# Kernel tuning notes

Hardware: AMD Instinct MI355X
Metric: run time of the kernel (lower is better)

## Reference

```python
import jax, jax.numpy as jnp
import numpy as np

D_MODEL = 1024
N_HEADS = 16
SEQ = 512  # == max_seq_len; rel-pos bias requires n_token == max_seq_len


def setup_inputs() -> dict:
    key = jax.random.key(0)
    ks = jax.random.split(key, 12)
    B = 16
    x = jax.random.normal(ks[0], (B, SEQ, D_MODEL), dtype=jnp.float32)
    c = jax.random.normal(ks[1], (B, SEQ, 8), dtype=jnp.float32)  # unused by forward
    s = 1.0 / np.sqrt(D_MODEL)
    Wq = jax.random.normal(ks[2], (D_MODEL, D_MODEL), dtype=jnp.float32) * s
    bq = jnp.zeros((D_MODEL,), dtype=jnp.float32)
    Wk = jax.random.normal(ks[3], (D_MODEL, D_MODEL), dtype=jnp.float32) * s
    bk = jnp.zeros((D_MODEL,), dtype=jnp.float32)
    Wv = jax.random.normal(ks[4], (D_MODEL, D_MODEL), dtype=jnp.float32) * s
    bv = jnp.zeros((D_MODEL,), dtype=jnp.float32)
    Wo = jax.random.normal(ks[5], (D_MODEL, D_MODEL), dtype=jnp.float32) * s
    bo = jnp.zeros((D_MODEL,), dtype=jnp.float32)
    # trunc_normal_(std=0.02) approximated by normal*0.02 (values stay small)
    rel_table = jax.random.normal(ks[6], (2 * SEQ - 1, N_HEADS), dtype=jnp.float32) * 0.02
    return {"x": x, "c": c, "Wq": Wq, "bq": bq, "Wk": Wk, "bk": bk,
            "Wv": Wv, "bv": bv, "Wo": Wo, "bo": bo, "rel_table": rel_table}


def reference(x, c, Wq, bq, Wk, bk, Wv, bv, Wo, bo, rel_table):
    # x: [B, S, D]; c is unused in the original forward
    B, S, D = x.shape
    H = N_HEADS
    dk = D // H
    scale = 1.0 / np.sqrt(dk)

    q = (x @ Wq + bq).reshape(B, S, H, dk)
    k = (x @ Wk + bk).reshape(B, S, H, dk)
    v = (x @ Wv + bv).reshape(B, S, H, dk)

    # scores: [B, H, S, S]
    scores = jnp.einsum('bihd,bjhd->bhij', q, k) * scale

    # relative position bias: index[i,j] = i + (S-1-j), values in [0, 2S-2]
    rel_index = jnp.arange(S)[:, None] + jnp.arange(S - 1, -1, -1)[None, :]  # [S,S]
    bias = rel_table[rel_index]            # [S, S, H]
    scores = scores + jnp.transpose(bias, (2, 0, 1))[None]  # [1,H,S,S]

    # causal_mask=False: original adds False * -1e9 == 0, so no mask term
    probs = jax.nn.softmax(scores, axis=-1)

    out = jnp.einsum('bhij,bjhd->bihd', probs, v).reshape(B, S, D)
    return out @ Wo + bo
```

## Files before the change

kernel.cpp:

```cpp
#include <hip/hip_runtime.h>
#include <hip/hip_bf16.h>
#include <stdint.h>

#define D_MODEL 1024
#define NH 16
#define SEQ 512
#define DK 64
#define BATCH 16
#define M_TOT (BATCH*SEQ)

typedef unsigned short u16;
typedef unsigned int u32;
typedef __attribute__((ext_vector_type(8))) __bf16 bf16x8;
typedef __attribute__((ext_vector_type(4))) u16 ushort4v;
typedef __attribute__((ext_vector_type(4))) float f32x4;

static __device__ __forceinline__ u16 f2bf(float f) {
    union { float f; u32 i; } c; c.f = f;
    return (u16)((c.i + 0x8000u) >> 16);
}
static __device__ __forceinline__ void async_copy16(const void* g, void* l) {
    __builtin_amdgcn_global_load_lds(
        (const __attribute__((address_space(1))) u32*)g,
        (__attribute__((address_space(3))) u32*)l, 16, 0, 0);
}
static __device__ __forceinline__ float fexp2(float x) {
    float r; asm("v_exp_f32 %0, %1" : "=v"(r) : "v"(x)); return r;
}

__global__ __launch_bounds__(256) void prep(const float* __restrict__ x,
                                            u16* __restrict__ xbf,
                                            const float* __restrict__ Wq,
                                            const float* __restrict__ Wk,
                                            const float* __restrict__ Wv,
                                            u16* __restrict__ Wt3) {
    __shared__ u16 tile[64][65];
    const int bid = blockIdx.x;
    const int t = threadIdx.x;
    if (bid < 2048) {
        #pragma unroll
        for (int it = 0; it < 4; ++it) {
            const int i = (bid * 1024 + it * 256 + t) * 4;
            float4 v = *(const float4*)&x[i];
            ushort4v o;
            o[0] = f2bf(v.x); o[1] = f2bf(v.y); o[2] = f2bf(v.z); o[3] = f2bf(v.w);
            *(ushort4v*)&xbf[i] = o;
        }
        return;
    }
    const int tw = bid - 2048;
    const int z = tw >> 8;
    const float* W = (z == 0) ? Wq : (z == 1) ? Wk : Wv;
    const int n0 = (tw & 15) * 64, k0 = ((tw >> 4) & 15) * 64;
    #pragma unroll
    for (int p = 0; p < 16; ++p) {
        int idx = p * 256 + t;
        int r = idx >> 6, c = idx & 63;
        tile[r][c] = f2bf(W[(size_t)(k0 + r) * D_MODEL + (n0 + c)]);
    }
    __syncthreads();
    #pragma unroll
    for (int p = 0; p < 16; ++p) {
        int idx = p * 256 + t;
        int r = idx >> 6, c = idx & 63;
        Wt3[((size_t)z * D_MODEL + n0 + r) * D_MODEL + (k0 + c)] = tile[c][r];
    }
}

__global__ __launch_bounds__(256) void gemm_bt(const u16* __restrict__ A,
                                               const u16* __restrict__ Bt,
                                               const float* __restrict__ b0,
                                               const float* __restrict__ b1,
                                               const float* __restrict__ b2,
                                               void* __restrict__ o0,
                                               void* __restrict__ o1,
                                               void* __restrict__ o2,
                                               int qkv) {
    __shared__ __attribute__((aligned(16))) u16 smem[16896];
    u16* Asm = smem;
    u16* Bsm = smem + 8192;
    const int t = threadIdx.x;
    const int m0 = blockIdx.y * 128, n0 = blockIdx.x * 128;
    const int lane = t & 63, w = t >> 6;
    const int lm = lane & 15, quad = lane >> 4;
    const int wm = w >> 1, wn = w & 1;

    f32x4 acc[4][4];
    #pragma unroll
    for (int i = 0; i < 4; ++i)
        #pragma unroll
        for (int j = 0; j < 4; ++j) acc[i][j] = (f32x4){0.f, 0.f, 0.f, 0.f};

    for (int kt = 0; kt < D_MODEL / 64; ++kt) {
        const int k0 = kt * 64;
        __syncthreads();
        #pragma unroll
        for (int i = 0; i < 4; ++i) {
            int chunk = i * 256 + t;
            int row = chunk >> 3, c = chunk & 7;
            int cs = c ^ (row & 7);
            async_copy16(A + (size_t)(m0 + row) * D_MODEL + k0 + cs * 8, &Asm[chunk * 8]);
        }
        #pragma unroll
        for (int i = 0; i < 4; ++i) {
            int chunk = i * 256 + t;
            int row = chunk >> 3, c = chunk & 7;
            int cs = c ^ (row & 7);
            async_copy16(Bt + (size_t)(n0 + row) * D_MODEL + k0 + cs * 8, &Bsm[chunk * 8]);
        }
        __syncthreads();
        #pragma unroll
        for (int ks = 0; ks < 64; ks += 32) {
            const int cbase = ks >> 3;
            bf16x8 af[4], bfv[4];
            #pragma unroll
            for (int im = 0; im < 4; ++im) {
                const int row = wm * 64 + im * 16 + lm;
                const int c = (cbase + quad) ^ (row & 7);
                af[im] = *(const bf16x8*)&Asm[row * 64 + c * 8];
            }
            #pragma unroll
            for (int in = 0; in < 4; ++in) {
                const int row = wn * 64 + in * 16 + lm;
                const int c = (cbase + quad) ^ (row & 7);
                bfv[in] = *(const bf16x8*)&Bsm[row * 64 + c * 8];
            }
            #pragma unroll
            for (int im = 0; im < 4; ++im)
                #pragma unroll
                for (int in = 0; in < 4; ++in)
                    acc[im][in] = __builtin_amdgcn_mfma_f32_16x16x32_bf16(
                        af[im], bfv[in], acc[im][in], 0, 0, 0);
        }
    }

    __syncthreads();
    if (qkv) {
        const int sel = n0 >> 10;
        if (sel == 2) {
            #pragma unroll
            for (int in = 0; in < 4; ++in) {
                const int nn = (n0 & 1023) + wn * 64 + in * 16 + lm;
                const float bv = b2[nn];
                const int h = nn >> 6, d = nn & 63;
                #pragma unroll
                for (int im = 0; im < 4; ++im) {
                    const int mb = m0 + wm * 64 + im * 16 + quad * 4;
                    const int b = mb >> 9, s = mb & 511;
                    ushort4v pk;
                    #pragma unroll
                    for (int r = 0; r < 4; ++r) pk[r] = f2bf(acc[im][in][r] + bv);
                    *(ushort4v*)&((u16*)o2)[((size_t)(b * NH + h) * DK + d) * SEQ + s] = pk;
                }
            }
        } else {
            u16* dst = sel ? (u16*)o1 : (u16*)o0;
            const float* bb = sel ? b1 : b0;
            u16 (*Cs)[132] = (u16(*)[132])smem;
            #pragma unroll
            for (int in = 0; in < 4; ++in) {
                const int nl = wn * 64 + in * 16 + lm;
                const float bv = bb[(n0 & 1023) + nl];
                #pragma unroll
                for (int im = 0; im < 4; ++im)
                    #pragma unroll
                    for (int r = 0; r < 4; ++r)
                        Cs[wm * 64 + im * 16 + quad * 4 + r][nl] =
                            f2bf(acc[im][in][r] + bv);
            }
            __syncthreads();
            const int rr = t >> 1, hh = t & 1;
            const int m = m0 + rr;
            const int b = m >> 9, s = m & 511;
            const int h = ((n0 & 1023) >> 6) + hh;
            u16* dp = &dst[((size_t)(b * NH + h) * SEQ + s) * DK];
            #pragma unroll
            for (int c = 0; c < 8; ++c)
                *(uint4*)&dp[c * 8] = *(const uint4*)&Cs[rr][hh * 64 + c * 8];
        }
    } else {
        float (*Cs)[132] = (float(*)[132])smem;
        #pragma unroll
        for (int ph = 0; ph < 2; ++ph) {
            if (wm == ph) {
                #pragma unroll
                for (int in = 0; in < 4; ++in) {
                    const int nl = wn * 64 + in * 16 + lm;
                    const float bv = b0[n0 + nl];
                    #pragma unroll
                    for (int im = 0; im < 4; ++im)
                        #pragma unroll
                        for (int r = 0; r < 4; ++r)
                            Cs[im * 16 + quad * 4 + r][nl] = acc[im][in][r] + bv;
                }
            }
            __syncthreads();
            const int rr = t >> 2, qq = t & 3;
            float* dp = &((float*)o0)[(size_t)(m0 + ph * 64 + rr) * D_MODEL + n0 + qq * 32];
            #pragma unroll
            for (int c = 0; c < 8; ++c)
                *(uint4*)&dp[c * 4] = *(const uint4*)&Cs[rr][qq * 32 + c * 4];
            __syncthreads();
        }
    }
}

__global__ __launch_bounds__(256) void attn_flash(const u16* __restrict__ qg,
                                                  const u16* __restrict__ kg,
                                                  const u16* __restrict__ vTg,
                                                  const float* __restrict__ rel,
                                                  u16* __restrict__ aout,
                                                  const float* __restrict__ Wo,
                                                  u16* __restrict__ WtO) {
    __shared__ __attribute__((aligned(16))) u16 qt[128 * 64];
    __shared__ __attribute__((aligned(16))) u16 Pl[4][32][72];
    __shared__ __attribute__((aligned(16))) float bcs[4][648];

    const int t = threadIdx.x;
    const int F = blockIdx.x;
    if (F >= 1024) {
        u16 (*tile)[65] = (u16(*)[65])qt;
        const int tw = F - 1024;
        const int n0 = (tw & 15) * 64, k0 = (tw >> 4) * 64;
        #pragma unroll
        for (int p = 0; p < 16; ++p) {
            int idx = p * 256 + t;
            int r = idx >> 6, c = idx & 63;
            tile[r][c] = f2bf(Wo[(size_t)(k0 + r) * D_MODEL + (n0 + c)]);
        }
        __syncthreads();
        #pragma unroll
        for (int p = 0; p < 16; ++p) {
            int idx = p * 256 + t;
            int r = idx >> 6, c = idx & 63;
            WtO[(size_t)(n0 + r) * D_MODEL + (k0 + c)] = tile[c][r];
        }
        return;
    }

    const int lane = t & 63, w = t >> 6;
    const int lm = lane & 15, quad = lane >> 4;
    const int xcd = F & 7, qti = (F >> 3) & 3, grp = F >> 5;
    const int p = grp * 8 + xcd;
    const int h = p & 15, b = p >> 4;
    const int q0 = qti * 128;
    const size_t bh = (size_t)(b * NH + h);
    const u16* qb = qg + bh * SEQ * DK;
    const u16* kb = kg + bh * SEQ * DK;
    const u16* vb = vTg + bh * DK * SEQ;

    #pragma unroll
    for (int i = 0; i < 4; ++i) {
        const int chunk = i * 256 + t, row = chunk >> 3, c = chunk & 7;
        const int cs = c ^ (row & 7);
        *(uint4*)&qt[chunk * 8] = *(const uint4*)&qb[(q0 + row) * DK + cs * 8];
    }
    for (int u = t; u < 639; u += 256) {
        const float bv = rel[(q0 + u) * NH + h] * 1.44269504f;
        #pragma unroll
        for (int c = 0; c < 4; ++c) bcs[c][u + 4 - c] = bv;
    }

    __syncthreads();

    bf16x8 aq[2][2];
    #pragma unroll
    for (int g = 0; g < 2; ++g) {
        const int ra = w * 32 + g * 16 + lm;
        aq[g][0] = *(const bf16x8*)&qt[ra * 64 + ((quad) ^ (ra & 7)) * 8];
        aq[g][1] = *(const bf16x8*)&qt[ra * 64 + ((4 + quad) ^ (ra & 7)) * 8];
    }

    float lsum[2] = {0.f, 0.f};
    f32x4 o[2][4];
    #pragma unroll
    for (int g = 0; g < 2; ++g)
        #pragma unroll
        for (int sd = 0; sd < 4; ++sd) o[g][sd] = (f32x4){0.f, 0.f, 0.f, 0.f};

    const float scale2 = 0.125f * 1.44269504f;
    const int cc = lm & 3;
    const int abase = w * 32 + lm + 512 - quad * 4 - cc;

    for (int jt = 0; jt < 8; ++jt) {
        const int j0 = jt * 64;

        #pragma unroll
        for (int js = 0; js < 4; ++js) {
            const u16* kp = kb + (size_t)(j0 + js * 16 + lm) * DK;
            bf16x8 bk0 = *(const bf16x8*)&kp[quad * 8];
            bf16x8 bk1 = *(const bf16x8*)&kp[32 + quad * 8];
            #pragma unroll
            for (int g = 0; g < 2; ++g) {
                f32x4 c = (f32x4){0.f, 0.f, 0.f, 0.f};
                c = __builtin_amdgcn_mfma_f32_16x16x32_bf16(bk0, aq[g][0], c, 0, 0, 0);
                c = __builtin_amdgcn_mfma_f32_16x16x32_bf16(bk1, aq[g][1], c, 0, 0, 0);
                const f32x4 bc4 = *(const f32x4*)&bcs[cc][abase + g * 16 - j0 - js * 16];
                ushort4v pk;
                #pragma unroll
                for (int r = 0; r < 4; ++r) {
                    float e = fexp2(c[r] * scale2 + bc4[3 - r]);
                    lsum[g] += e;
                    pk[r] = f2bf(e);
                }
                *(ushort4v*)&Pl[w][g * 16 + lm][js * 16 + quad * 4] = pk;
            }
        }

        bf16x8 ap[2][2];
        #pragma unroll
        for (int g = 0; g < 2; ++g) {
            ap[g][0] = *(const bf16x8*)&Pl[w][g * 16 + lm][quad * 8];
            ap[g][1] = *(const bf16x8*)&Pl[w][g * 16 + lm][32 + quad * 8];
        }
        #pragma unroll
        for (int sd = 0; sd < 4; ++sd) {
            const u16* vp = vb + (size_t)(sd * 16 + lm) * SEQ + j0;
            bf16x8 bv0 = *(const bf16x8*)&vp[quad * 8];
            bf16x8 bv1 = *(const bf16x8*)&vp[32 + quad * 8];
            #pragma unroll
            for (int g = 0; g < 2; ++g) {
                o[g][sd] = __builtin_amdgcn_mfma_f32_16x16x32_bf16(bv0, ap[g][0], o[g][sd], 0, 0, 0);
                o[g][sd] = __builtin_amdgcn_mfma_f32_16x16x32_bf16(bv1, ap[g][1], o[g][sd], 0, 0, 0);
            }
        }
    }

    #pragma unroll
    for (int g = 0; g < 2; ++g) {
        float s = lsum[g];
        s += __shfl_xor(s, 16, 64);
        s += __shfl_xor(s, 32, 64);
        const float rinv = 1.0f / s;
        #pragma unroll
        for (int sd = 0; sd < 4; ++sd) {
            ushort4v pk;
            #pragma unroll
            for (int r = 0; r < 4; ++r) pk[r] = f2bf(o[g][sd][r] * rinv);
            *(ushort4v*)&Pl[w][g * 16 + lm][sd * 16 + quad * 4] = pk;
        }
    }
    const int rowl = lane >> 1, ch = lane & 1;
    u16* dp = aout + (size_t)(b * SEQ + q0 + w * 32 + rowl) * D_MODEL + h * DK + ch * 32;
    #pragma unroll
    for (int c = 0; c < 4; ++c)
        *(uint4*)&dp[c * 8] = *(const uint4*)&Pl[w][rowl][ch * 32 + c * 8];
}

extern "C" void kernel_launch(void* const* d_in, const int* in_sizes, int n_in,
                              void* d_out, int out_size, void* d_ws, size_t ws_size,
                              hipStream_t stream) {
    const float* x   = (const float*)d_in[0];
    const float* Wq  = (const float*)d_in[2];
    const float* bq  = (const float*)d_in[3];
    const float* Wk  = (const float*)d_in[4];
    const float* bk  = (const float*)d_in[5];
    const float* Wv  = (const float*)d_in[6];
    const float* bv  = (const float*)d_in[7];
    const float* Wo  = (const float*)d_in[8];
    const float* bo  = (const float*)d_in[9];
    const float* rel = (const float*)d_in[10];
    float* out = (float*)d_out;

    u16* ws = (u16*)d_ws;
    const size_t WSZ = (size_t)D_MODEL * D_MODEL;
    const size_t TSZ = (size_t)M_TOT * D_MODEL;
    u16* Wt3 = ws;
    u16* xbf = Wt3 + 3 * WSZ;
    u16* qws = xbf + TSZ;
    u16* kws = qws + TSZ;
    u16* vws = kws + TSZ;
    u16* aws = xbf;

    dim3 tb(256);
    prep<<<dim3(2048 + 768), tb, 0, stream>>>(x, xbf, Wq, Wk, Wv, Wt3);
    gemm_bt<<<dim3(24, 64), tb, 0, stream>>>(xbf, Wt3, bq, bk, bv, qws, kws, vws, 1);
    attn_flash<<<dim3(1024 + 256), tb, 0, stream>>>(qws, kws, vws, rel, aws, Wo, Wt3);
    gemm_bt<<<dim3(8, 64), tb, 0, stream>>>(aws, Wt3, bo, nullptr, nullptr,
                                            (void*)out, nullptr, nullptr, 0);
}
```

Before: 291.5 us.

## Double-buffer K/V tiles in LDS with async copies and MFMA row sums

The attention kernel now stages K and V^T tiles into double-buffered LDS with async global-to-LDS copies. The next tile is prefetched while the current one is computed, replacing direct global loads inside the inner loop. The softmax denominator is accumulated by an MFMA against a ones vector instead of scalar adds plus shuffles. Bias is stored once rather than four shifted copies, and bf16 packing uses the hardware v_cvt_pk_bf16_f32. The trade-offs are more LDS per block (possibly lower occupancy), an extra barrier per tile, and a row sum computed from bf16-rounded probabilities.

```diff
diff --git a/kernel.cpp b/kernel.cpp
--- a/kernel.cpp
+++ b/kernel.cpp
@@ -18,6 +18,9 @@
 static __device__ __forceinline__ u16 f2bf(float f) {
     union { float f; u32 i; } c; c.f = f;
     return (u16)((c.i + 0x8000u) >> 16);
+}
+static __device__ __forceinline__ u32 cvtpk(float lo, float hi) {
+    u32 r; asm("v_cvt_pk_bf16_f32 %0, %1, %2" : "=v"(r) : "v"(lo), "v"(hi)); return r;
 }
 static __device__ __forceinline__ void async_copy16(const void* g, void* l) {
     __builtin_amdgcn_global_load_lds(
@@ -212,14 +215,17 @@
                                                   u16* __restrict__ aout,
                                                   const float* __restrict__ Wo,
                                                   u16* __restrict__ WtO) {
-    __shared__ __attribute__((aligned(16))) u16 qt[128 * 64];
-    __shared__ __attribute__((aligned(16))) u16 Pl[4][32][72];
-    __shared__ __attribute__((aligned(16))) float bcs[4][648];
+    __shared__ __attribute__((aligned(16))) char smem_raw[53760];
+    u16* ktb = (u16*)smem_raw;
+    u16* vtb = (u16*)(smem_raw + 16384);
+    float* biasb = (float*)(smem_raw + 32768);
+    u16* qt = (u16*)(smem_raw + 35328);
+    u16 (*Pl)[32][72] = (u16(*)[32][72])(smem_raw + 35328);
 
     const int t = threadIdx.x;
     const int F = blockIdx.x;
     if (F >= 1024) {
-        u16 (*tile)[65] = (u16(*)[65])qt;
+        u16 (*tile)[65] = (u16(*)[65])smem_raw;
         const int tw = F - 1024;
         const int n0 = (tw & 15) * 64, k0 = (tw >> 4) * 64;
         #pragma unroll
@@ -250,16 +256,20 @@
     const u16* vb = vTg + bh * DK * SEQ;
 
     #pragma unroll
+    for (int i = 0; i < 2; ++i) {
+        const int chunk = i * 256 + t, row = chunk >> 3, c = chunk & 7;
+        const int cs = c ^ (row & 7);
+        async_copy16(kb + row * DK + cs * 8, &ktb[chunk * 8]);
+        async_copy16(vb + row * SEQ + cs * 8, &vtb[chunk * 8]);
+    }
+
+    #pragma unroll
     for (int i = 0; i < 4; ++i) {
         const int chunk = i * 256 + t, row = chunk >> 3, c = chunk & 7;
         const int cs = c ^ (row & 7);
         *(uint4*)&qt[chunk * 8] = *(const uint4*)&qb[(q0 + row) * DK + cs * 8];
     }
-    for (int u = t; u < 639; u += 256) {
-        const float bv = rel[(q0 + u) * NH + h] * 1.44269504f;
-        #pragma unroll
-        for (int c = 0; c < 4; ++c) bcs[c][u + 4 - c] = bv;
-    }
+    for (int u = t; u < 639; u += 256) biasb[u] = rel[(q0 + u) * NH + h] * 1.44269504f;
 
     __syncthreads();
 
@@ -270,40 +280,59 @@
         aq[g][0] = *(const bf16x8*)&qt[ra * 64 + ((quad) ^ (ra & 7)) * 8];
         aq[g][1] = *(const bf16x8*)&qt[ra * 64 + ((4 + quad) ^ (ra & 7)) * 8];
     }
-
-    float lsum[2] = {0.f, 0.f};
+    __syncthreads();
+
+    bf16x8 ones;
+    #pragma unroll
+    for (int i = 0; i < 8; ++i) ones[i] = (__bf16)1.0f;
+
+    f32x4 ol[2];
     f32x4 o[2][4];
     #pragma unroll
-    for (int g = 0; g < 2; ++g)
+    for (int g = 0; g < 2; ++g) {
+        ol[g] = (f32x4){0.f, 0.f, 0.f, 0.f};
         #pragma unroll
         for (int sd = 0; sd < 4; ++sd) o[g][sd] = (f32x4){0.f, 0.f, 0.f, 0.f};
+    }
 
     const float scale2 = 0.125f * 1.44269504f;
-    const int cc = lm & 3;
-    const int abase = w * 32 + lm + 512 - quad * 4 - cc;
 
     for (int jt = 0; jt < 8; ++jt) {
+        if (jt) __syncthreads();
+        const int cur = jt & 1, nxt = cur ^ 1;
+        u16* ktc = ktb + cur * 4096;
+        u16* vtc = vtb + cur * 4096;
+        if (jt < 7) {
+            const int j1 = (jt + 1) * 64;
+            u16* ktn = ktb + nxt * 4096;
+            u16* vtn = vtb + nxt * 4096;
+            #pragma unroll
+            for (int i = 0; i < 2; ++i) {
+                const int chunk = i * 256 + t, row = chunk >> 3, c = chunk & 7;
+                const int cs = c ^ (row & 7);
+                async_copy16(kb + (j1 + row) * DK + cs * 8, &ktn[chunk * 8]);
+                async_copy16(vb + row * SEQ + j1 + cs * 8, &vtn[chunk * 8]);
+            }
+        }
         const int j0 = jt * 64;
 
         #pragma unroll
         for (int js = 0; js < 4; ++js) {
-            const u16* kp = kb + (size_t)(j0 + js * 16 + lm) * DK;
-            bf16x8 bk0 = *(const bf16x8*)&kp[quad * 8];
-            bf16x8 bk1 = *(const bf16x8*)&kp[32 + quad * 8];
+            const int rb = js * 16 + lm;
+            bf16x8 bk0 = *(const bf16x8*)&ktc[rb * 64 + ((quad) ^ (rb & 7)) * 8];
+            bf16x8 bk1 = *(const bf16x8*)&ktc[rb * 64 + ((4 + quad) ^ (rb & 7)) * 8];
             #pragma unroll
             for (int g = 0; g < 2; ++g) {
                 f32x4 c = (f32x4){0.f, 0.f, 0.f, 0.f};
                 c = __builtin_amdgcn_mfma_f32_16x16x32_bf16(bk0, aq[g][0], c, 0, 0, 0);
                 c = __builtin_amdgcn_mfma_f32_16x16x32_bf16(bk1, aq[g][1], c, 0, 0, 0);
-                const f32x4 bc4 = *(const f32x4*)&bcs[cc][abase + g * 16 - j0 - js * 16];
-                ushort4v pk;
-                #pragma unroll
-                for (int r = 0; r < 4; ++r) {
-                    float e = fexp2(c[r] * scale2 + bc4[3 - r]);
-                    lsum[g] += e;
-                    pk[r] = f2bf(e);
-                }
-                *(ushort4v*)&Pl[w][g * 16 + lm][js * 16 + quad * 4] = pk;
+                const int bb0 = w * 32 + g * 16 + lm + 511 - j0 - js * 16 - quad * 4;
+                float e0 = fexp2(c[0] * scale2 + biasb[bb0]);
+                float e1 = fexp2(c[1] * scale2 + biasb[bb0 - 1]);
+                float e2 = fexp2(c[2] * scale2 + biasb[bb0 - 2]);
+                float e3 = fexp2(c[3] * scale2 + biasb[bb0 - 3]);
+                uint2 pk = {cvtpk(e0, e1), cvtpk(e2, e3)};
+                *(uint2*)&Pl[w][g * 16 + lm][js * 16 + quad * 4] = pk;
             }
         }
 
@@ -312,12 +341,14 @@
         for (int g = 0; g < 2; ++g) {
             ap[g][0] = *(const bf16x8*)&Pl[w][g * 16 + lm][quad * 8];
             ap[g][1] = *(const bf16x8*)&Pl[w][g * 16 + lm][32 + quad * 8];
+            ol[g] = __builtin_amdgcn_mfma_f32_16x16x32_bf16(ones, ap[g][0], ol[g], 0, 0, 0);
+            ol[g] = __builtin_amdgcn_mfma_f32_16x16x32_bf16(ones, ap[g][1], ol[g], 0, 0, 0);
         }
         #pragma unroll
         for (int sd = 0; sd < 4; ++sd) {
-            const u16* vp = vb + (size_t)(sd * 16 + lm) * SEQ + j0;
-            bf16x8 bv0 = *(const bf16x8*)&vp[quad * 8];
-            bf16x8 bv1 = *(const bf16x8*)&vp[32 + quad * 8];
+            const int rv = sd * 16 + lm;
+            bf16x8 bv0 = *(const bf16x8*)&vtc[rv * 64 + ((quad) ^ (rv & 7)) * 8];
+            bf16x8 bv1 = *(const bf16x8*)&vtc[rv * 64 + ((4 + quad) ^ (rv & 7)) * 8];
             #pragma unroll
             for (int g = 0; g < 2; ++g) {
                 o[g][sd] = __builtin_amdgcn_mfma_f32_16x16x32_bf16(bv0, ap[g][0], o[g][sd], 0, 0, 0);
@@ -328,16 +359,12 @@
 
     #pragma unroll
     for (int g = 0; g < 2; ++g) {
-        float s = lsum[g];
-        s += __shfl_xor(s, 16, 64);
-        s += __shfl_xor(s, 32, 64);
-        const float rinv = 1.0f / s;
+        const float rinv = 1.0f / ol[g][0];
         #pragma unroll
         for (int sd = 0; sd < 4; ++sd) {
-            ushort4v pk;
-            #pragma unroll
-            for (int r = 0; r < 4; ++r) pk[r] = f2bf(o[g][sd][r] * rinv);
-            *(ushort4v*)&Pl[w][g * 16 + lm][sd * 16 + quad * 4] = pk;
+            uint2 pk = {cvtpk(o[g][sd][0] * rinv, o[g][sd][1] * rinv),
+                        cvtpk(o[g][sd][2] * rinv, o[g][sd][3] * rinv)};
+            *(uint2*)&Pl[w][g * 16 + lm][sd * 16 + quad * 4] = pk;
         }
     }
     const int rowl = lane >> 1, ch = lane & 1;
```

Measured after the change: 245.8 us, median of 2. 15.7% less time.
